# Kernel optimization log

Hardware: AMD Instinct MI355X
Metric: run time of the kernel (lower is better)

The kernel has to match this reference:

```python
import jax, jax.numpy as jnp
import numpy as np

ENT_SIZE = 100000; REL_SIZE = 500; ENT_DIM = 256; REL_DIM = 256; H = 256
E = 2048; S = 32; N = 1024; THRESHOLD = 1.0; EPS = 1e-5


def _xav(k, shape):
    fan_in = shape[-1]
    fan_out = shape[-2] if len(shape) > 1 else shape[-1]
    std = (2.0 / (fan_in + fan_out)) ** 0.5
    return jax.random.normal(k, shape, jnp.float32) * std


def setup_inputs() -> dict:
    key = jax.random.key(0)
    ks = jax.random.split(key, 16)
    inp = {}
    inp["neighbors"] = jax.random.randint(ks[0], (E, S), 0, ENT_SIZE)
    inp["pos_h"] = jax.random.randint(ks[1], (N,), 0, E)
    inp["pos_t"] = jax.random.randint(ks[2], (N,), 0, E)
    inp["pos_r"] = jax.random.randint(ks[3], (N,), 0, REL_SIZE)
    inp["neg_h"] = jax.random.randint(ks[4], (N,), 0, E)
    inp["neg_t"] = jax.random.randint(ks[5], (N,), 0, E)
    inp["neg_r"] = jax.random.randint(ks[6], (N,), 0, REL_SIZE)
    inp["ent_embed"] = _xav(ks[7], (ENT_SIZE + 1, ENT_DIM))
    inp["rel_embed"] = _xav(ks[8], (REL_SIZE, REL_DIM))
    inp["trans"] = _xav(ks[9], (2 * REL_SIZE, REL_DIM, ENT_DIM))
    inp["W_ih_f"] = _xav(ks[10], (4 * H, ENT_DIM)); inp["W_hh_f"] = _xav(ks[11], (4 * H, H))
    inp["W_ih_b"] = _xav(ks[12], (4 * H, ENT_DIM)); inp["W_hh_b"] = _xav(ks[13], (4 * H, H))
    inp["b_f"] = jnp.zeros((4 * H,), jnp.float32)
    inp["b_b"] = jnp.zeros((4 * H,), jnp.float32)
    inp["W_lin"] = _xav(ks[14], (ENT_DIM, 2 * H)); inp["b_lin"] = jnp.zeros((ENT_DIM,), jnp.float32)
    inp["gamma"] = jnp.ones((ENT_DIM,), jnp.float32); inp["beta"] = jnp.zeros((ENT_DIM,), jnp.float32)
    return inp


def _lstm_final(x, W_ih, W_hh, b):
    # x: [E,S,D] -> final hidden state [E,H] (PyTorch LSTM gate order i,f,g,o; b = b_ih+b_hh)
    h0 = jnp.zeros((x.shape[0], H), x.dtype)
    def step(carry, xt):
        h, c = carry
        g = xt @ W_ih.T + h @ W_hh.T + b  # [E,4H]
        i, f, gg, o = jnp.split(g, 4, axis=-1)
        c = jax.nn.sigmoid(f) * c + jax.nn.sigmoid(i) * jnp.tanh(gg)
        h = jax.nn.sigmoid(o) * jnp.tanh(c)
        return (h, c), None
    (h, _), _ = jax.lax.scan(step, (h0, h0), jnp.swapaxes(x, 0, 1))
    return h


def _context(ent_embed, neighbors, W_ih_f, W_hh_f, b_f, W_ih_b, W_hh_b, b_b, W_lin, b_lin, gamma, beta):
    x_seq = ent_embed[neighbors]  # [E,S,D]
    h_f = _lstm_final(x_seq, W_ih_f, W_hh_f, b_f)
    h_b = _lstm_final(x_seq[:, ::-1], W_ih_b, W_hh_b, b_b)
    lin = jnp.concatenate([h_f, h_b], -1) @ W_lin.T + b_lin  # [E,ENT_DIM]
    # BatchNorm1d in training mode: batch stats (biased variance)
    mu = lin.mean(0)
    var = lin.var(0)
    return jnp.tanh(gamma * (lin - mu) * jax.lax.rsqrt(var + EPS) + beta)


def _score(trans, rel_embed, ctx, h_idx, r_idx, t_idx):
    Wh = trans[r_idx]             # [N,REL_DIM,ENT_DIM] (grouped expert GEMV, batched)
    Wt = trans[r_idx + REL_SIZE]
    d = jnp.einsum('nre,ne->nr', Wh, ctx[h_idx]) - jnp.einsum('nre,ne->nr', Wt, ctx[t_idx])
    return jnp.linalg.norm(d + rel_embed[r_idx], axis=1)


def reference(neighbors, pos_h, pos_t, pos_r, neg_h, neg_t, neg_r,
              ent_embed, rel_embed, trans, W_ih_f, W_hh_f, W_ih_b, W_hh_b,
              b_f, b_b, W_lin, b_lin, gamma, beta):
    ctx = _context(ent_embed, neighbors, W_ih_f, W_hh_f, b_f, W_ih_b, W_hh_b, b_b,
                   W_lin, b_lin, gamma, beta)
    pos_n = _score(trans, rel_embed, ctx, pos_h, pos_r, pos_t)
    neg_n = _score(trans, rel_embed, ctx, neg_h, neg_r, neg_t)
    return jnp.sum(pos_n + jax.nn.relu(THRESHOLD - neg_n))
```

## Files before the change

### kernel.cpp

```cpp
#include <hip/hip_runtime.h>

constexpr int kE   = 2048;
constexpr int kS   = 32;
constexpr int kD   = 256;
constexpr int kK   = 512;
constexpr int kREL = 500;
constexpr int kN   = 1024;

typedef unsigned short u16;
typedef __attribute__((ext_vector_type(8))) _Float16 f16x8;
typedef __attribute__((ext_vector_type(4))) float    f32x4;
typedef __attribute__((ext_vector_type(4))) unsigned short us4;

static __device__ __forceinline__ u16 f2h(float f) {
  _Float16 h = (_Float16)f;
  return __builtin_bit_cast(u16, h);
}
static __device__ __forceinline__ float h2f(u16 v) {
  _Float16 h = __builtin_bit_cast(_Float16, v);
  return (float)h;
}
static __device__ __forceinline__ float sigf(float x) { return 1.f / (1.f + __expf(-x)); }
static __device__ __forceinline__ float tanhfast(float x) {
  float e = __expf(2.f * x);
  return 1.f - 2.f / (e + 1.f);
}
static __device__ __forceinline__ void gl_lds16(const void* g, void* l) {
  __builtin_amdgcn_global_load_lds((const __attribute__((address_space(1))) unsigned int*)g,
                                   (__attribute__((address_space(3))) unsigned int*)l, 16, 0, 0);
}

__global__ void prep_gather(const float* __restrict__ Wih_f, const float* __restrict__ Whh_f,
                            const float* __restrict__ Wih_b, const float* __restrict__ Whh_b,
                            const float* __restrict__ Wlin_in,
                            const int* __restrict__ neighbors, const float* __restrict__ ent,
                            u16* __restrict__ Wv3, u16* __restrict__ Whhr,
                            u16* __restrict__ Wlin, u16* __restrict__ ximg) {
  if (blockIdx.x < 576) {
    int idx = blockIdx.x * 256 + threadIdx.x;
    if (idx < 65536) {
      int q  = idx & 2047;
      int ch = (idx >> 11) & 3;
      int y  = (idx >> 13) & 3;
      int d  = idx >> 15;
      int j  = q >> 3;
      int k8 = (q & 7) ^ (j & 7);
      int jg = y * 256 + j;
      int g = (jg >> 4) & 3, u = (jg >> 6) * 16 + (jg & 15);
      int R = g * 256 + u;
      int k = ch * 64 + k8 * 8;
      const float* src = (d ? Wih_b : Wih_f) + R * 256 + k;
      ushort oa[8];
#pragma unroll
      for (int i = 0; i < 8; i++) oa[i] = f2h(src[i]);
      *(uint4*)((char*)Wv3 + (size_t)idx * 16) = *(uint4*)oa;
    } else if (idx < 131072) {
      int i2 = idx - 65536;
      int d = i2 >> 15;
      int j = (i2 & 32767) >> 5;
      int k = (i2 & 31) * 8;
      int g = (j >> 4) & 3, u = (j >> 6) * 16 + (j & 15);
      int R = g * 256 + u;
      const float* src = (d ? Whh_b : Whh_f) + R * 256 + k;
      ushort oa[8];
#pragma unroll
      for (int i = 0; i < 8; i++) oa[i] = f2h(src[i]);
      *(uint4*)((char*)Whhr + (size_t)i2 * 16) = *(uint4*)oa;
    } else if (idx < 131072 + 16384) {
      int q = (idx - 131072) * 8;
#pragma unroll
      for (int i = 0; i < 8; i++) Wlin[q + i] = f2h(Wlin_in[q + i]);
    }
  } else {
    int idx = (blockIdx.x - 576) * 256 + threadIdx.x;
    int q    = idx & 511;
    int ch   = (idx >> 9) & 3;
    int tile = (idx >> 11) & 31;
    int s    = idx >> 16;
    int row = q >> 3;
    int c8 = (q & 7) ^ (row & 7);
    int e = tile * 64 + row;
    int k = ch * 64 + c8 * 8;
    int nb = neighbors[e * 32 + s];
    const float* src = ent + (size_t)nb * 256 + k;
    float4 v0 = *(const float4*)src;
    float4 v1 = *(const float4*)(src + 4);
    ushort oa[8];
    oa[0] = f2h(v0.x); oa[1] = f2h(v0.y); oa[2] = f2h(v0.z); oa[3] = f2h(v0.w);
    oa[4] = f2h(v1.x); oa[5] = f2h(v1.y); oa[6] = f2h(v1.z); oa[7] = f2h(v1.w);
    *(uint4*)((char*)ximg + (size_t)idx * 16) = *(uint4*)oa;
  }
}

static __device__ __forceinline__ void xgemm_body(
    const u16* __restrict__ ximg, const u16* __restrict__ Wv3,
    const float* __restrict__ b_f, const float* __restrict__ b_b,
    u16* __restrict__ gx, int ts, int etile, int y, int dir,
    char* As, char* Bs) {
  const int tid = threadIdx.x, lane = tid & 63, w = tid >> 6;
  const int l15 = lane & 15, lq = lane >> 4;
  const int e0 = etile * 64;
  const int s = dir ? (31 - ts) : ts;
  const char* imgA = (const char*)ximg + (size_t)(s * 32 + etile) * 32768;
  const char* imgB = (const char*)Wv3 + (size_t)(dir * 4 + y) * 131072;
  const float* bd = dir ? b_b : b_f;
  const int u = (y * 4 + w) * 16 + l15;

  f32x4 acc[4][4];
#pragma unroll
  for (int n = 0; n < 4; n++) {
    float bv = bd[n * 256 + u];
#pragma unroll
    for (int m = 0; m < 4; m++) acc[m][n] = (f32x4){bv, bv, bv, bv};
  }

  for (int ch = 0; ch < 4; ++ch) {
#pragma unroll
    for (int i = 0; i < 2; i++)
      gl_lds16(imgA + ch * 8192 + i * 4096 + w * 1024 + lane * 16,
               As + i * 4096 + w * 1024);
#pragma unroll
    for (int i = 0; i < 8; i++)
      gl_lds16(imgB + (size_t)ch * 32768 + i * 4096 + w * 1024 + lane * 16,
               Bs + i * 4096 + w * 1024);
    __syncthreads();
#pragma unroll
    for (int ks = 0; ks < 2; ++ks) {
      const int kb = ks * 64 + lq * 16;
      f16x8 a[4], b[4];
#pragma unroll
      for (int m = 0; m < 4; m++) {
        int row = m * 16 + l15;
        a[m] = *(const f16x8*)(As + row * 128 + (kb ^ ((row & 7) << 4)));
      }
#pragma unroll
      for (int n = 0; n < 4; n++) {
        int row = w * 64 + n * 16 + l15;
        b[n] = *(const f16x8*)(Bs + row * 128 + (kb ^ ((row & 7) << 4)));
      }
#pragma unroll
      for (int m = 0; m < 4; m++)
#pragma unroll
        for (int n = 0; n < 4; n++)
          acc[m][n] = __builtin_amdgcn_mfma_f32_16x16x32_f16(a[m], b[n], acc[m][n], 0, 0, 0);
    }
    __syncthreads();
  }

  u16* out = gx + ((size_t)(dir * 2 + (ts & 1)) * kE) * 1024;
#pragma unroll
  for (int m = 0; m < 4; m++)
#pragma unroll
    for (int r = 0; r < 4; r++) {
      int e = e0 + m * 16 + lq * 4 + r;
      us4 o;
      o[0] = f2h(acc[m][0][r]); o[1] = f2h(acc[m][1][r]);
      o[2] = f2h(acc[m][2][r]); o[3] = f2h(acc[m][3][r]);
      *(us4*)(out + ((size_t)e * 256 + u) * 4) = o;
    }
}

static __device__ __forceinline__ void rec_body(
    const u16* __restrict__ gx, const u16* __restrict__ Whhr,
    const u16* __restrict__ hprev, u16* __restrict__ hnext,
    float* __restrict__ cbuf, int t, int bid) {
  const int tid = threadIdx.x, lane = tid & 63, w = tid >> 6;
  const int l15 = lane & 15, lq = lane >> 4;
  const int dir = bid >> 8;
  const int rem = bid & 255;
  const int jg = rem >> 6;
  const int et = rem & 63;
  const int e0 = et * 32;
  const int c0 = jg * 256 + w * 64;
  const int unit = (c0 >> 6) * 16 + l15;

  const u16* Wd  = Whhr + ((size_t)dir * 1024 + c0) * kD;
  const u16* hpd = hprev + (size_t)dir * kE * kD;
  u16* hnd = hnext + (size_t)dir * kE * kD;
  float* cd = cbuf + (size_t)dir * kE * kD;
  const u16* gp = gx + ((size_t)(dir * 2 + (t & 1)) * kE) * 1024;

  f32x4 acc[2][4];
#pragma unroll
  for (int m = 0; m < 2; m++)
#pragma unroll
    for (int r = 0; r < 4; r++) {
      us4 g = *(const us4*)(gp + (size_t)(e0 + m * 16 + lq * 4 + r) * 1024 + unit * 4);
#pragma unroll
      for (int n = 0; n < 4; n++) acc[m][n][r] = h2f(g[n]);
    }

  const int klane = lq * 8;
#pragma unroll
  for (int ks = 0; ks < 8; ks++) {
    const int ka = ks * 32 + klane;
    f16x8 a[2], b[4];
#pragma unroll
    for (int m = 0; m < 2; m++)
      a[m] = *(const f16x8*)(hpd + (size_t)(e0 + m * 16 + l15) * kD + ka);
#pragma unroll
    for (int n = 0; n < 4; n++)
      b[n] = *(const f16x8*)(Wd + (size_t)(n * 16 + l15) * kD + ka);
#pragma unroll
    for (int m = 0; m < 2; m++)
#pragma unroll
      for (int n = 0; n < 4; n++)
        acc[m][n] = __builtin_amdgcn_mfma_f32_16x16x32_f16(a[m], b[n], acc[m][n], 0, 0, 0);
  }

#pragma unroll
  for (int m = 0; m < 2; m++)
#pragma unroll
    for (int r = 0; r < 4; r++) {
      int row = e0 + m * 16 + lq * 4 + r;
      size_t off = (size_t)row * kD + unit;
      float gi = acc[m][0][r];
      float gf = acc[m][1][r];
      float gg = acc[m][2][r];
      float go = acc[m][3][r];
      float c_old = cd[off];
      float cn = sigf(gf) * c_old + sigf(gi) * tanhfast(gg);
      cd[off] = cn;
      hnd[off] = f2h(sigf(go) * tanhfast(cn));
    }
}

__global__ __launch_bounds__(256) void step_fused(
    const u16* __restrict__ ximg, const u16* __restrict__ Wv3,
    const float* __restrict__ b_f, const float* __restrict__ b_b,
    u16* __restrict__ gx, const u16* __restrict__ Whhr,
    const u16* __restrict__ hprev, u16* __restrict__ hnext,
    float* __restrict__ cbuf, int t) {
  __shared__ __align__(16) char As[8192];
  __shared__ __align__(16) char Bs[32768];
  if (blockIdx.x < 512) {
    rec_body(gx, Whhr, hprev, hnext, cbuf, t, blockIdx.x);
  } else {
    int ts = t + 1;
    if (ts >= kS) return;
    int b = blockIdx.x - 512;
    xgemm_body(ximg, Wv3, b_f, b_b, gx, ts, b & 31, (b >> 5) & 3, b >> 7, As, Bs);
  }
}

__global__ __launch_bounds__(256) void xgemm_pro(
    const u16* __restrict__ ximg, const u16* __restrict__ Wv3,
    const float* __restrict__ b_f, const float* __restrict__ b_b,
    u16* __restrict__ gx) {
  __shared__ __align__(16) char As[8192];
  __shared__ __align__(16) char Bs[32768];
  int b = blockIdx.x;
  xgemm_body(ximg, Wv3, b_f, b_b, gx, 0, b & 31, (b >> 5) & 3, b >> 7, As, Bs);
}

static __device__ __forceinline__ void gemm_tile(
    const u16* __restrict__ Alo, const u16* __restrict__ Ahi,
    const u16* __restrict__ W, int e0,
    u16* As, u16* Bs, f32x4 (&acc)[4][4]) {
  const int tid = threadIdx.x;
  const int lane = tid & 63;
  const int w = tid >> 6;
#pragma unroll
  for (int m = 0; m < 4; m++)
#pragma unroll
    for (int n = 0; n < 4; n++) acc[m][n] = (f32x4){0.f, 0.f, 0.f, 0.f};

  for (int ch = 0; ch < 8; ++ch) {
    const int k0 = ch * 64;
    __syncthreads();
    const u16* Asrc = (k0 < 256) ? Alo : Ahi;
    const int kbase = (k0 < 256) ? k0 : (k0 - 256);
#pragma unroll
    for (int i = 0; i < 2; i++) {
      int idx = tid + i * 256;
      int row = idx >> 3, c8 = idx & 7;
      uint4 v = *(const uint4*)(Asrc + (size_t)(e0 + row) * 256 + kbase + c8 * 8);
      *(uint4*)((char*)As + row * 128 + ((c8 * 16) ^ ((row & 7) << 4))) = v;
    }
#pragma unroll
    for (int i = 0; i < 8; i++) {
      int idx = tid + i * 256;
      int j = idx >> 3, c8 = idx & 7;
      uint4 v = *(const uint4*)(W + (size_t)j * kK + k0 + c8 * 8);
      *(uint4*)((char*)Bs + j * 128 + ((c8 * 16) ^ ((j & 7) << 4))) = v;
    }
    __syncthreads();
#pragma unroll
    for (int ks = 0; ks < 2; ++ks) {
      const int kb = ks * 64 + (lane >> 4) * 16;
      f16x8 a[4], b[4];
#pragma unroll
      for (int m = 0; m < 4; m++) {
        int row = m * 16 + (lane & 15);
        a[m] = *(const f16x8*)((const char*)As + row * 128 + (kb ^ ((row & 7) << 4)));
      }
#pragma unroll
      for (int n = 0; n < 4; n++) {
        int row = w * 64 + n * 16 + (lane & 15);
        b[n] = *(const f16x8*)((const char*)Bs + row * 128 + (kb ^ ((row & 7) << 4)));
      }
#pragma unroll
      for (int m = 0; m < 4; m++)
#pragma unroll
        for (int n = 0; n < 4; n++)
          acc[m][n] = __builtin_amdgcn_mfma_f32_16x16x32_f16(a[m], b[n], acc[m][n], 0, 0, 0);
    }
  }
}

__global__ __launch_bounds__(256) void lin_kernel(
    const u16* __restrict__ hf, const u16* __restrict__ hb,
    const u16* __restrict__ Wl, const float* __restrict__ b_lin,
    float* __restrict__ lin, float* __restrict__ part) {
  __shared__ __align__(16) char smem[40960];
  u16* As = (u16*)smem;
  u16* Bs = (u16*)(smem + 8192);
  const int tid = threadIdx.x, lane = tid & 63, w = tid >> 6;
  const int l15 = lane & 15, lq = lane >> 4;
  const int e0 = blockIdx.x * 64;
  f32x4 acc[4][4];
  gemm_tile(hf, hb, Wl, e0, As, Bs, acc);
#pragma unroll
  for (int n = 0; n < 4; n++) {
    int col = w * 64 + n * 16 + l15;
    float bl = b_lin[col];
    float s1 = 0.f, s2 = 0.f;
#pragma unroll
    for (int m = 0; m < 4; m++)
#pragma unroll
      for (int r = 0; r < 4; r++) {
        int e = e0 + m * 16 + lq * 4 + r;
        float v = acc[m][n][r] + bl;
        lin[(size_t)e * 256 + col] = v;
        s1 += v; s2 += v * v;
      }
    s1 += __shfl_down(s1, 16); s2 += __shfl_down(s2, 16);
    s1 += __shfl_down(s1, 32); s2 += __shfl_down(s2, 32);
    if (lq == 0) {
      part[blockIdx.x * 256 + col] = s1;
      part[8192 + blockIdx.x * 256 + col] = s2;
    }
  }
}

__global__ void bn_apply(const float* __restrict__ lin, const float* __restrict__ part,
                         const float* __restrict__ gamma, const float* __restrict__ beta,
                         float* __restrict__ ctx) {
  int c = threadIdx.x;
  float s = 0.f, s2 = 0.f;
  for (int b = 0; b < 32; b++) { s += part[b * 256 + c]; s2 += part[8192 + b * 256 + c]; }
  float mu = s * (1.f / 2048.f);
  float rsig = rsqrtf(s2 * (1.f / 2048.f) - mu * mu + 1e-5f);
  float ga = gamma[c], be = beta[c];
  int e0 = blockIdx.x * 8;
  for (int e = e0; e < e0 + 8; ++e) {
    float x = lin[(size_t)e * 256 + c];
    ctx[(size_t)e * 256 + c] = tanhf(ga * (x - mu) * rsig + be);
  }
}

__global__ void group_rel(const int* __restrict__ pr, const int* __restrict__ nr,
                          int* __restrict__ offs, int* __restrict__ list) {
  __shared__ int cnt[512], sc[512], cur[512];
  int tid = threadIdx.x;
  cnt[tid] = 0;
  __syncthreads();
  for (int i = tid; i < 2 * kN; i += 512) {
    int r = (i < kN) ? pr[i] : nr[i - kN];
    atomicAdd(&cnt[r], 1);
  }
  __syncthreads();
  sc[tid] = cnt[tid];
  __syncthreads();
  for (int d = 1; d < 512; d <<= 1) {
    int v = (tid >= d) ? sc[tid - d] : 0;
    __syncthreads();
    sc[tid] += v;
    __syncthreads();
  }
  int excl = (tid == 0) ? 0 : sc[tid - 1];
  cur[tid] = excl;
  if (tid <= kREL) offs[tid] = excl;
  __syncthreads();
  for (int i = tid; i < 2 * kN; i += 512) {
    int r = (i < kN) ? pr[i] : nr[i - kN];
    int p = atomicAdd(&cur[r], 1);
    list[p] = i;
  }
}

__global__ __launch_bounds__(256) void score_grouped(
    const float* __restrict__ ctx, const float* __restrict__ trans,
    const float* __restrict__ rel_embed,
    const int* __restrict__ ph, const int* __restrict__ pt,
    const int* __restrict__ nh, const int* __restrict__ nt,
    const int* __restrict__ offs, const int* __restrict__ list,
    float* __restrict__ scores) {
  int r = blockIdx.x;
  int start = offs[r], end = offs[r + 1];
  if (start >= end) return;
  int tid = threadIdx.x;
  __shared__ float cs[8][2][256];
  __shared__ float red[8][4];
  float relv = rel_embed[r * 256 + tid];
  const float4* Whp = (const float4*)(trans + (size_t)r * 65536 + (size_t)tid * 256);
  const float4* Wtp = (const float4*)(trans + ((size_t)r + kREL) * 65536 + (size_t)tid * 256);

  for (int chunk = start; chunk < end; chunk += 8) {
    int G = min(8, end - chunk);
    for (int j = 0; j < G; j++) {
      int i = list[chunk + j];
      int hh = (i < kN) ? ph[i] : nh[i - kN];
      int tt = (i < kN) ? pt[i] : nt[i - kN];
      cs[j][0][tid] = ctx[(size_t)hh * 256 + tid];
      cs[j][1][tid] = ctx[(size_t)tt * 256 + tid];
    }
    __syncthreads();
    float acc[8];
#pragma unroll
    for (int j = 0; j < 8; j++) acc[j] = relv;
#pragma unroll 2
    for (int q = 0; q < 64; q++) {
      float4 w1 = Whp[q];
      float4 w2 = Wtp[q];
#pragma unroll
      for (int j = 0; j < 8; j++) {
        float4 xh = *(const float4*)&cs[j][0][q * 4];
        float4 xt = *(const float4*)&cs[j][1][q * 4];
        acc[j] += w1.x * xh.x + w1.y * xh.y + w1.z * xh.z + w1.w * xh.w
                - (w2.x * xt.x + w2.y * xt.y + w2.z * xt.z + w2.w * xt.w);
      }
    }
    for (int j = 0; j < G; j++) {
      float sq = acc[j] * acc[j];
      for (int o = 32; o; o >>= 1) sq += __shfl_down(sq, o);
      if ((tid & 63) == 0) red[j][tid >> 6] = sq;
    }
    __syncthreads();
    if (tid < G) {
      float s = red[tid][0] + red[tid][1] + red[tid][2] + red[tid][3];
      scores[list[chunk + tid]] = sqrtf(s);
    }
    __syncthreads();
  }
}

__global__ void final_reduce(const float* __restrict__ scores, float* __restrict__ out) {
  int tid = threadIdx.x;
  float a = 0.f;
  for (int i = tid; i < 2 * kN; i += 256) {
    float s = scores[i];
    a += (i < kN) ? s : fmaxf(0.f, 1.f - s);
  }
  for (int off = 32; off; off >>= 1) a += __shfl_down(a, off);
  __shared__ float w4[4];
  if ((tid & 63) == 0) w4[tid >> 6] = a;
  __syncthreads();
  if (tid == 0) out[0] = w4[0] + w4[1] + w4[2] + w4[3];
}

extern "C" void kernel_launch(void* const* d_in, const int* in_sizes, int n_in,
                              void* d_out, int out_size, void* d_ws, size_t ws_size,
                              hipStream_t stream) {
  const int*   neighbors = (const int*)d_in[0];
  const int*   pos_h = (const int*)d_in[1];
  const int*   pos_t = (const int*)d_in[2];
  const int*   pos_r = (const int*)d_in[3];
  const int*   neg_h = (const int*)d_in[4];
  const int*   neg_t = (const int*)d_in[5];
  const int*   neg_r = (const int*)d_in[6];
  const float* ent_embed = (const float*)d_in[7];
  const float* rel_embed = (const float*)d_in[8];
  const float* trans = (const float*)d_in[9];
  const float* W_ih_f = (const float*)d_in[10];
  const float* W_hh_f = (const float*)d_in[11];
  const float* W_ih_b = (const float*)d_in[12];
  const float* W_hh_b = (const float*)d_in[13];
  const float* b_f = (const float*)d_in[14];
  const float* b_b = (const float*)d_in[15];
  const float* W_lin = (const float*)d_in[16];
  const float* b_lin = (const float*)d_in[17];
  const float* gamma = (const float*)d_in[18];
  const float* beta = (const float*)d_in[19];

  char* ws = (char*)d_ws;
  size_t off = 0;
  auto alloc = [&](size_t bytes) {
    void* p = ws + off;
    off = (off + bytes + 255) & ~(size_t)255;
    return p;
  };
  u16* Wv3    = (u16*)alloc((size_t)65536 * 16);
  u16* Whhr   = (u16*)alloc((size_t)2 * 1024 * kD * 2);
  u16* Wlin   = (u16*)alloc((size_t)256 * kK * 2);
  u16* ximg   = (u16*)alloc((size_t)2097152 * 16);
  u16* h0     = (u16*)alloc((size_t)2 * kE * kD * 2);
  u16* h1     = (u16*)alloc((size_t)2 * kE * kD * 2);
  float* cbuf = (float*)alloc((size_t)2 * kE * kD * 4);
  u16* gx     = (u16*)alloc((size_t)2 * 2 * kE * 1024 * 2);
  float* lin  = (float*)alloc((size_t)kE * 256 * 4);
  float* part = (float*)alloc((size_t)2 * 32 * 256 * 4);
  float* ctx  = (float*)alloc((size_t)kE * 256 * 4);
  float* scores = (float*)alloc((size_t)2 * kN * 4);
  int* offsb  = (int*)alloc((size_t)512 * 4);
  int* list   = (int*)alloc((size_t)2 * kN * 4);
  (void)in_sizes; (void)n_in; (void)out_size; (void)ws_size;

  hipMemsetAsync(h0, 0, (size_t)2 * kE * kD * 2, stream);
  hipMemsetAsync(cbuf, 0, (size_t)2 * kE * kD * 4, stream);

  prep_gather<<<576 + 8192, 256, 0, stream>>>(W_ih_f, W_hh_f, W_ih_b, W_hh_b, W_lin,
                                              neighbors, ent_embed,
                                              Wv3, Whhr, Wlin, ximg);
  group_rel<<<1, 512, 0, stream>>>(pos_r, neg_r, offsb, list);
  xgemm_pro<<<256, 256, 0, stream>>>(ximg, Wv3, b_f, b_b, gx);

  for (int t = 0; t < kS; t++) {
    const u16* hp = (t & 1) ? h1 : h0;
    u16* hn = (t & 1) ? h0 : h1;
    step_fused<<<768, 256, 0, stream>>>(ximg, Wv3, b_f, b_b, gx, Whhr, hp, hn, cbuf, t);
  }

  lin_kernel<<<32, 256, 0, stream>>>(h0, h0 + (size_t)kE * kD, Wlin, b_lin, lin, part);
  bn_apply<<<256, 256, 0, stream>>>(lin, part, gamma, beta, ctx);
  score_grouped<<<kREL, 256, 0, stream>>>(ctx, trans, rel_embed,
                                          pos_h, pos_t, neg_h, neg_t, offsb, list, scores);
  final_reduce<<<1, 256, 0, stream>>>(scores, (float*)d_out);
}
```

Baseline: 870.7 us.

## Hoist input-gate GEMM out of recurrence and split scoring across row halves

The input projection for all 32 timesteps now runs as one large GEMM before the recurrence, storing the full gate buffer instead of double-buffering it inside the fused per-step kernel. The per-step kernel now does only the recurrent part over 512 blocks. The gate buffer is written and read with nontemporal stores and loads. Scoring is split into two blocks per relation that each handle 128 output rows, processing up to 16 triples per chunk with templated widths and accumulating squared norms atomically, with the square root taken in the final reduce. This trades a much larger gate buffer (256 MB) and extra memory traffic for fewer wasted xgemm blocks per step and more scoring parallelism.

```diff
diff --git a/kernel.cpp b/kernel.cpp
--- a/kernel.cpp
+++ b/kernel.cpp
@@ -92,13 +92,17 @@
   }
 }
 
-static __device__ __forceinline__ void xgemm_body(
+__global__ __launch_bounds__(256) void xgemm(
     const u16* __restrict__ ximg, const u16* __restrict__ Wv3,
     const float* __restrict__ b_f, const float* __restrict__ b_b,
-    u16* __restrict__ gx, int ts, int etile, int y, int dir,
-    char* As, char* Bs) {
+    u16* __restrict__ gx) {
+  __shared__ __align__(16) char As[8192];
+  __shared__ __align__(16) char Bs[32768];
   const int tid = threadIdx.x, lane = tid & 63, w = tid >> 6;
   const int l15 = lane & 15, lq = lane >> 4;
+  const int ts = blockIdx.x >> 5;
+  const int etile = blockIdx.x & 31;
+  const int y = blockIdx.y, dir = blockIdx.z;
   const int e0 = etile * 64;
   const int s = dir ? (31 - ts) : ts;
   const char* imgA = (const char*)ximg + (size_t)(s * 32 + etile) * 32768;
@@ -147,7 +151,7 @@
     __syncthreads();
   }
 
-  u16* out = gx + ((size_t)(dir * 2 + (ts & 1)) * kE) * 1024;
+  u16* out = gx + ((size_t)(dir * kS + ts) * kE) * 1024;
 #pragma unroll
   for (int m = 0; m < 4; m++)
 #pragma unroll
@@ -156,16 +160,17 @@
       us4 o;
       o[0] = f2h(acc[m][0][r]); o[1] = f2h(acc[m][1][r]);
       o[2] = f2h(acc[m][2][r]); o[3] = f2h(acc[m][3][r]);
-      *(us4*)(out + ((size_t)e * 256 + u) * 4) = o;
-    }
-}
-
-static __device__ __forceinline__ void rec_body(
+      __builtin_nontemporal_store(o, (us4*)(out + ((size_t)e * 256 + u) * 4));
+    }
+}
+
+__global__ __launch_bounds__(256) void lstm_step(
     const u16* __restrict__ gx, const u16* __restrict__ Whhr,
     const u16* __restrict__ hprev, u16* __restrict__ hnext,
-    float* __restrict__ cbuf, int t, int bid) {
+    float* __restrict__ cbuf, int t) {
   const int tid = threadIdx.x, lane = tid & 63, w = tid >> 6;
   const int l15 = lane & 15, lq = lane >> 4;
+  const int bid = blockIdx.x;
   const int dir = bid >> 8;
   const int rem = bid & 255;
   const int jg = rem >> 6;
@@ -178,14 +183,15 @@
   const u16* hpd = hprev + (size_t)dir * kE * kD;
   u16* hnd = hnext + (size_t)dir * kE * kD;
   float* cd = cbuf + (size_t)dir * kE * kD;
-  const u16* gp = gx + ((size_t)(dir * 2 + (t & 1)) * kE) * 1024;
+  const u16* gp = gx + ((size_t)(dir * kS + t) * kE) * 1024;
 
   f32x4 acc[2][4];
 #pragma unroll
   for (int m = 0; m < 2; m++)
 #pragma unroll
     for (int r = 0; r < 4; r++) {
-      us4 g = *(const us4*)(gp + (size_t)(e0 + m * 16 + lq * 4 + r) * 1024 + unit * 4);
+      us4 g = __builtin_nontemporal_load(
+          (const us4*)(gp + (size_t)(e0 + m * 16 + lq * 4 + r) * 1024 + unit * 4));
 #pragma unroll
       for (int n = 0; n < 4; n++) acc[m][n][r] = h2f(g[n]);
     }
@@ -223,34 +229,6 @@
       cd[off] = cn;
       hnd[off] = f2h(sigf(go) * tanhfast(cn));
     }
-}
-
-__global__ __launch_bounds__(256) void step_fused(
-    const u16* __restrict__ ximg, const u16* __restrict__ Wv3,
-    const float* __restrict__ b_f, const float* __restrict__ b_b,
-    u16* __restrict__ gx, const u16* __restrict__ Whhr,
-    const u16* __restrict__ hprev, u16* __restrict__ hnext,
-    float* __restrict__ cbuf, int t) {
-  __shared__ __align__(16) char As[8192];
-  __shared__ __align__(16) char Bs[32768];
-  if (blockIdx.x < 512) {
-    rec_body(gx, Whhr, hprev, hnext, cbuf, t, blockIdx.x);
-  } else {
-    int ts = t + 1;
-    if (ts >= kS) return;
-    int b = blockIdx.x - 512;
-    xgemm_body(ximg, Wv3, b_f, b_b, gx, ts, b & 31, (b >> 5) & 3, b >> 7, As, Bs);
-  }
-}
-
-__global__ __launch_bounds__(256) void xgemm_pro(
-    const u16* __restrict__ ximg, const u16* __restrict__ Wv3,
-    const float* __restrict__ b_f, const float* __restrict__ b_b,
-    u16* __restrict__ gx) {
-  __shared__ __align__(16) char As[8192];
-  __shared__ __align__(16) char Bs[32768];
-  int b = blockIdx.x;
-  xgemm_body(ximg, Wv3, b_f, b_b, gx, 0, b & 31, (b >> 5) & 3, b >> 7, As, Bs);
 }
 
 static __device__ __forceinline__ void gemm_tile(
@@ -389,67 +367,111 @@
   }
 }
 
+template <int NJ>
+static __device__ __forceinline__ void score_body(
+    const float* __restrict__ ctx, const float* __restrict__ trans,
+    const float* __restrict__ rel_embed,
+    const int* __restrict__ ph, const int* __restrict__ pt,
+    const int* __restrict__ nh, const int* __restrict__ nt,
+    const int* __restrict__ list, float* __restrict__ sqacc,
+    int r, int half, int start, int G,
+    float* csh, float* cst, float (*red)[4], int* tidx) {
+  const int tid = threadIdx.x;
+#pragma unroll
+  for (int j = 0; j < NJ; j++) {
+    float vh = 0.f, vt = 0.f;
+    if (j < G) {
+      int i = list[start + j];
+      int hh = (i < kN) ? ph[i] : nh[i - kN];
+      int tt = (i < kN) ? pt[i] : nt[i - kN];
+      vh = ctx[(size_t)hh * 256 + tid];
+      vt = ctx[(size_t)tt * 256 + tid];
+      if (tid == 0) tidx[j] = i;
+    }
+    csh[j * 256 + tid] = vh;
+    cst[j * 256 + tid] = vt;
+  }
+  __syncthreads();
+
+  const int row = half * 128 + (tid >> 1);
+  const int q4b = (tid & 1) * 32;
+  const float4* whp = (const float4*)(trans + (size_t)r * 65536 + (size_t)row * 256) + q4b;
+  const float4* wtp = (const float4*)(trans + ((size_t)r + kREL) * 65536 + (size_t)row * 256) + q4b;
+  const float4* ch4 = (const float4*)csh;
+  const float4* ct4 = (const float4*)cst;
+
+  float acc[NJ];
+#pragma unroll
+  for (int j = 0; j < NJ; j++) acc[j] = 0.f;
+
+  for (int line = 0; line < 4; line++) {
+    float4 wh[8], wt[8];
+#pragma unroll
+    for (int i = 0; i < 8; i++) { wh[i] = whp[line * 8 + i]; wt[i] = wtp[line * 8 + i]; }
+#pragma unroll
+    for (int q4 = 0; q4 < 8; q4++) {
+      const int qa = q4b + line * 8 + q4;
+#pragma unroll
+      for (int j = 0; j < NJ; j++) {
+        float4 xh = ch4[j * 64 + qa];
+        float4 xt = ct4[j * 64 + qa];
+        acc[j] += wh[q4].x * xh.x + wh[q4].y * xh.y + wh[q4].z * xh.z + wh[q4].w * xh.w
+                - (wt[q4].x * xt.x + wt[q4].y * xt.y + wt[q4].z * xt.z + wt[q4].w * xt.w);
+      }
+    }
+  }
+
+  const float rv = rel_embed[r * 256 + row];
+#pragma unroll
+  for (int j = 0; j < NJ; j++) {
+    float d = acc[j] + __shfl_xor(acc[j], 1) + rv;
+    float v = d * d;
+    v += __shfl_down(v, 32); v += __shfl_down(v, 16);
+    v += __shfl_down(v, 8);  v += __shfl_down(v, 4);
+    v += __shfl_down(v, 2);  v += __shfl_down(v, 1);
+    if ((tid & 63) == 0) red[j][tid >> 6] = v;
+  }
+  __syncthreads();
+  if (tid < G) {
+    float s = (red[tid][0] + red[tid][1] + red[tid][2] + red[tid][3]) * 0.5f;
+    atomicAdd(&sqacc[tidx[tid]], s);
+  }
+  __syncthreads();
+}
+
 __global__ __launch_bounds__(256) void score_grouped(
     const float* __restrict__ ctx, const float* __restrict__ trans,
     const float* __restrict__ rel_embed,
     const int* __restrict__ ph, const int* __restrict__ pt,
     const int* __restrict__ nh, const int* __restrict__ nt,
     const int* __restrict__ offs, const int* __restrict__ list,
-    float* __restrict__ scores) {
-  int r = blockIdx.x;
+    float* __restrict__ sqacc) {
+  const int r = blockIdx.x >> 1, half = blockIdx.x & 1;
   int start = offs[r], end = offs[r + 1];
   if (start >= end) return;
-  int tid = threadIdx.x;
-  __shared__ float cs[8][2][256];
-  __shared__ float red[8][4];
-  float relv = rel_embed[r * 256 + tid];
-  const float4* Whp = (const float4*)(trans + (size_t)r * 65536 + (size_t)tid * 256);
-  const float4* Wtp = (const float4*)(trans + ((size_t)r + kREL) * 65536 + (size_t)tid * 256);
-
-  for (int chunk = start; chunk < end; chunk += 8) {
-    int G = min(8, end - chunk);
-    for (int j = 0; j < G; j++) {
-      int i = list[chunk + j];
-      int hh = (i < kN) ? ph[i] : nh[i - kN];
-      int tt = (i < kN) ? pt[i] : nt[i - kN];
-      cs[j][0][tid] = ctx[(size_t)hh * 256 + tid];
-      cs[j][1][tid] = ctx[(size_t)tt * 256 + tid];
-    }
-    __syncthreads();
-    float acc[8];
-#pragma unroll
-    for (int j = 0; j < 8; j++) acc[j] = relv;
-#pragma unroll 2
-    for (int q = 0; q < 64; q++) {
-      float4 w1 = Whp[q];
-      float4 w2 = Wtp[q];
-#pragma unroll
-      for (int j = 0; j < 8; j++) {
-        float4 xh = *(const float4*)&cs[j][0][q * 4];
-        float4 xt = *(const float4*)&cs[j][1][q * 4];
-        acc[j] += w1.x * xh.x + w1.y * xh.y + w1.z * xh.z + w1.w * xh.w
-                - (w2.x * xt.x + w2.y * xt.y + w2.z * xt.z + w2.w * xt.w);
-      }
-    }
-    for (int j = 0; j < G; j++) {
-      float sq = acc[j] * acc[j];
-      for (int o = 32; o; o >>= 1) sq += __shfl_down(sq, o);
-      if ((tid & 63) == 0) red[j][tid >> 6] = sq;
-    }
-    __syncthreads();
-    if (tid < G) {
-      float s = red[tid][0] + red[tid][1] + red[tid][2] + red[tid][3];
-      scores[list[chunk + tid]] = sqrtf(s);
-    }
-    __syncthreads();
-  }
-}
-
-__global__ void final_reduce(const float* __restrict__ scores, float* __restrict__ out) {
+  __shared__ float csh[16 * 256];
+  __shared__ float cst[16 * 256];
+  __shared__ float red[16][4];
+  __shared__ int tidx[16];
+  for (int c = start; c < end; c += 16) {
+    int G = min(16, end - c);
+    if (G <= 4)
+      score_body<4>(ctx, trans, rel_embed, ph, pt, nh, nt, list, sqacc, r, half, c, G,
+                    csh, cst, red, tidx);
+    else if (G <= 8)
+      score_body<8>(ctx, trans, rel_embed, ph, pt, nh, nt, list, sqacc, r, half, c, G,
+                    csh, cst, red, tidx);
+    else
+      score_body<16>(ctx, trans, rel_embed, ph, pt, nh, nt, list, sqacc, r, half, c, G,
+                     csh, cst, red, tidx);
+  }
+}
+
+__global__ void final_reduce(const float* __restrict__ sqacc, float* __restrict__ out) {
   int tid = threadIdx.x;
   float a = 0.f;
   for (int i = tid; i < 2 * kN; i += 256) {
-    float s = scores[i];
+    float s = sqrtf(sqacc[i]);
     a += (i < kN) ? s : fmaxf(0.f, 1.f - s);
   }
   for (int off = 32; off; off >>= 1) a += __shfl_down(a, off);
@@ -497,33 +519,35 @@
   u16* h0     = (u16*)alloc((size_t)2 * kE * kD * 2);
   u16* h1     = (u16*)alloc((size_t)2 * kE * kD * 2);
   float* cbuf = (float*)alloc((size_t)2 * kE * kD * 4);
-  u16* gx     = (u16*)alloc((size_t)2 * 2 * kE * 1024 * 2);
+  u16* gx     = (u16*)alloc((size_t)2 * kS * kE * 1024 * 2);
   float* lin  = (float*)alloc((size_t)kE * 256 * 4);
   float* part = (float*)alloc((size_t)2 * 32 * 256 * 4);
   float* ctx  = (float*)alloc((size_t)kE * 256 * 4);
-  float* scores = (float*)alloc((size_t)2 * kN * 4);
+  float* sqacc = (float*)alloc((size_t)2 * kN * 4);
   int* offsb  = (int*)alloc((size_t)512 * 4);
   int* list   = (int*)alloc((size_t)2 * kN * 4);
   (void)in_sizes; (void)n_in; (void)out_size; (void)ws_size;
 
   hipMemsetAsync(h0, 0, (size_t)2 * kE * kD * 2, stream);
   hipMemsetAsync(cbuf, 0, (size_t)2 * kE * kD * 4, stream);
+  hipMemsetAsync(sqacc, 0, (size_t)2 * kN * 4, stream);
 
   prep_gather<<<576 + 8192, 256, 0, stream>>>(W_ih_f, W_hh_f, W_ih_b, W_hh_b, W_lin,
                                               neighbors, ent_embed,
                                               Wv3, Whhr, Wlin, ximg);
   group_rel<<<1, 512, 0, stream>>>(pos_r, neg_r, offsb, list);
-  xgemm_pro<<<256, 256, 0, stream>>>(ximg, Wv3, b_f, b_b, gx);
+
+  xgemm<<<dim3(1024, 4, 2), 256, 0, stream>>>(ximg, Wv3, b_f, b_b, gx);
 
   for (int t = 0; t < kS; t++) {
     const u16* hp = (t & 1) ? h1 : h0;
     u16* hn = (t & 1) ? h0 : h1;
-    step_fused<<<768, 256, 0, stream>>>(ximg, Wv3, b_f, b_b, gx, Whhr, hp, hn, cbuf, t);
+    lstm_step<<<512, 256, 0, stream>>>(gx, Whhr, hp, hn, cbuf, t);
   }
 
   lin_kernel<<<32, 256, 0, stream>>>(h0, h0 + (size_t)kE * kD, Wlin, b_lin, lin, part);
   bn_apply<<<256, 256, 0, stream>>>(lin, part, gamma, beta, ctx);
-  score_grouped<<<kREL, 256, 0, stream>>>(ctx, trans, rel_embed,
-                                          pos_h, pos_t, neg_h, neg_t, offsb, list, scores);
-  final_reduce<<<1, 256, 0, stream>>>(scores, (float*)d_out);
-}
+  score_grouped<<<2 * kREL, 256, 0, stream>>>(ctx, trans, rel_embed,
+                                              pos_h, pos_t, neg_h, neg_t, offsb, list, sqacc);
+  final_reduce<<<1, 256, 0, stream>>>(sqacc, (float*)d_out);
+}
```

Result: faster. 804.9 us, median of 2 (-7.6%).
